# Performance work log

Hardware: AMD Instinct MI355X
Metric: run time of the kernel (lower is better)

The kernel has to match this reference:

```python
import jax, jax.numpy as jnp
import numpy as np

EMBED = 2048
HEADS = 16
HEAD_DIM = EMBED // HEADS
CHUNK = 128
BASE = 10000.0
EPS = 1e-6


def setup_inputs() -> dict:
    key = jax.random.key(0)
    ks = jax.random.split(key, 8)
    b, n, d = 2, 2048, EMBED
    std = 0.02
    return {
        "x": jax.random.normal(ks[0], (b, n, d), jnp.float32),
        "Wq": jax.random.normal(ks[1], (d, d), jnp.float32) * std,
        "Wk": jax.random.normal(ks[2], (d, d), jnp.float32) * std,
        "Wv": jax.random.normal(ks[3], (d, d), jnp.float32) * std,
        "Wo": jax.random.normal(ks[4], (d, d), jnp.float32) * std,
        "Wg1": jax.random.normal(ks[5], (d, HEAD_DIM), jnp.float32) * std,
        "Wg2": jax.random.normal(ks[6], (HEAD_DIM, d), jnp.float32) * std,
        "norm_weight": jnp.ones((d,), jnp.float32),
    }


def _alibi_log_decay(h):
    # lightning attention 'constant' decay: per-head ALiBi slope, log_lambda = -slope
    slopes = 2.0 ** (-8.0 * (jnp.arange(h, dtype=jnp.float32) + 1.0) / h)
    return -slopes  # [h]


def _lrpe_rotate(x):
    # RoPE-like rotation on head_dim (half-split), offset=0
    b, n, h, d = x.shape
    half = d // 2
    theta = BASE ** (-2.0 * jnp.arange(half, dtype=jnp.float32) / d)  # [half]
    ang = jnp.arange(n, dtype=jnp.float32)[:, None] * theta[None, :]  # [n, half]
    cos = jnp.cos(ang)[None, :, None, :]
    sin = jnp.sin(ang)[None, :, None, :]
    x1, x2 = x[..., :half], x[..., half:]
    return jnp.concatenate([x1 * cos - x2 * sin, x1 * sin + x2 * cos], axis=-1)


def _lightning_attn(q, k, v, log_lam):
    # chunk-recurrent linear attention with per-head exponential decay
    b, n, h, d = q.shape
    C = CHUNK
    nc = n // C
    qc = q.reshape(b, nc, C, h, d).transpose(1, 0, 2, 3, 4)  # [nc,b,C,h,d]
    kc = k.reshape(b, nc, C, h, d).transpose(1, 0, 2, 3, 4)
    vc = v.reshape(b, nc, C, h, d).transpose(1, 0, 2, 3, 4)
    i = jnp.arange(C, dtype=jnp.float32)
    diff = i[:, None] - i[None, :]  # [C,C]
    # intra-chunk decay mask D[h,t,s] = lambda_h^(t-s) for t>=s else 0
    D = jnp.where(diff[None] >= 0, jnp.exp(log_lam[:, None, None] * diff[None]), 0.0)
    decay_q = jnp.exp(log_lam[None, :] * (i[:, None] + 1.0))    # [C,h]
    decay_k = jnp.exp(log_lam[None, :] * (C - 1.0 - i[:, None]))  # [C,h]
    lam_C = jnp.exp(log_lam * C)  # [h]

    def step(S, qkv):
        qi, ki, vi = qkv  # [b,C,h,d]
        scores = jnp.einsum('bthd,bshd->bhts', qi, ki) * D[None]
        o_intra = jnp.einsum('bhts,bshd->bthd', scores, vi)
        o_inter = jnp.einsum('bthd,bhde->bthe', qi * decay_q[None, :, :, None], S)
        S_new = lam_C[None, :, None, None] * S + jnp.einsum(
            'bshd,bshe->bhde', ki * decay_k[None, :, :, None], vi)
        return S_new, o_intra + o_inter

    S0 = jnp.zeros((b, h, d, d), q.dtype)
    _, o = jax.lax.scan(step, S0, (qc, kc, vc))  # o: [nc,b,C,h,d]
    return o.transpose(1, 0, 2, 3, 4).reshape(b, n, h, d)


def _gated_group_rmsnorm(o, gate, weight):
    # gate_pos='pre', gate_act='sigmoid', num_groups=HEADS
    b, n, d = o.shape
    x = o * jax.nn.sigmoid(gate)
    xg = x.reshape(b, n, HEADS, HEAD_DIM)
    ms = jnp.mean(xg * xg, axis=-1, keepdims=True)
    xg = xg * jax.lax.rsqrt(ms + EPS)
    return xg.reshape(b, n, d) * weight


def reference(x, Wq, Wk, Wv, Wo, Wg1, Wg2, norm_weight):
    b, n, d = x.shape
    q = (x @ Wq).reshape(b, n, HEADS, HEAD_DIM)
    k = (x @ Wk).reshape(b, n, HEADS, HEAD_DIM)
    v = (x @ Wv).reshape(b, n, HEADS, HEAD_DIM)
    q = jax.nn.silu(q)
    k = jax.nn.silu(k)
    q = _lrpe_rotate(q)
    k = _lrpe_rotate(k)
    log_lam = _alibi_log_decay(HEADS)
    o = _lightning_attn(q, k, v, log_lam).reshape(b, n, d)
    gate = (x @ Wg1) @ Wg2
    o = _gated_group_rmsnorm(o, gate, norm_weight)
    return o @ Wo
```

## Files before the change

### kernel.cpp

```cpp
#include <hip/hip_runtime.h>


#define DEV __device__ __forceinline__
typedef unsigned short u16;
typedef __bf16 bf16x8 __attribute__((ext_vector_type(8)));
typedef float f32x4 __attribute__((ext_vector_type(4)));
typedef u16 u16x8 __attribute__((ext_vector_type(8)));

DEV u16 f2bf(float f) {
  unsigned u = __builtin_bit_cast(unsigned, f);
  u += 0x7fffu + ((u >> 16) & 1u);
  return (u16)(u >> 16);
}
DEV float bf2f(u16 h) {
  unsigned u = ((unsigned)h) << 16;
  return __builtin_bit_cast(float, u);
}
DEV void async16(const u16* g, u16* l) {
  __builtin_amdgcn_global_load_lds(
      (const __attribute__((address_space(1))) unsigned int*)g,
      (__attribute__((address_space(3))) unsigned int*)l, 16, 0, 0);
}

__global__ void convert_f32_bf16(const float* __restrict__ in, u16* __restrict__ out, long n) {
  long i = ((long)blockIdx.x * blockDim.x + threadIdx.x) * 4;
  if (i >= n) return;
  float4 v = *(const float4*)(in + i);
  ushort4 p;
  p.x = f2bf(v.x); p.y = f2bf(v.y); p.z = f2bf(v.z); p.w = f2bf(v.w);
  *(ushort4*)(out + i) = p;
}

__global__ void transpose_all(const float* __restrict__ Wq, const float* __restrict__ Wk,
                              const float* __restrict__ Wv, const float* __restrict__ Wo,
                              const float* __restrict__ Wg1, const float* __restrict__ Wg2,
                              u16* __restrict__ wtqkvg, u16* __restrict__ wot,
                              u16* __restrict__ wg2t) {
  __shared__ float t[32][33];
  int id = blockIdx.x;
  const float* in; u16* out; int K, N, bx, by;
  bool perm = false;
  if (id < 12288) {
    int w = id >> 12, tt = id & 4095;
    in = (w == 0) ? Wq : (w == 1) ? Wk : Wv;
    out = wtqkvg + (long)w * 2048 * 2048;
    K = 2048; N = 2048; bx = tt & 63; by = tt >> 6;
    perm = (w < 2);
  } else if (id < 16384) {
    int tt = id - 12288;
    in = Wo; out = wot; K = 2048; N = 2048; bx = tt & 63; by = tt >> 6;
  } else if (id < 16640) {
    int tt = id - 16384;
    in = Wg1; out = wtqkvg + 6144L * 2048; K = 2048; N = 128; bx = tt & 3; by = tt >> 2;
  } else {
    int tt = id - 16640;
    in = Wg2; out = wg2t; K = 128; N = 2048; bx = tt & 63; by = tt >> 6;
  }
  int c = threadIdx.x & 31, r0 = threadIdx.x >> 5;
  for (int r = r0; r < 32; r += 8)
    t[r][c] = in[(long)(by * 32 + r) * N + bx * 32 + c];
  __syncthreads();
  for (int r = r0; r < 32; r += 8) {
    int n = bx * 32 + r, nr = n;
    if (perm) {
      int h = n >> 7, j = n & 127, jj = j & 63, hi = j >> 6;
      nr = h * 128 + (jj & 15) + 32 * (jj >> 4) + 16 * hi;
    }
    out[(long)nr * K + by * 32 + c] = f2bf(t[c][r]);
  }
}

template <typename OutT>
__global__ __launch_bounds__(256, 2) void gemm_bt(
    const u16* __restrict__ A, const u16* __restrict__ B, OutT* __restrict__ C,
    int M, int N, int K, int lda, int ldb, int ldc, int rot,
    int nc, long sA1, long sA2, long sB1, long sB2, long sC1, long sC2) {
  __shared__ u16 sA[128 * 64], sB[128 * 64];
  {
    int z = blockIdx.z, z1 = z / nc, z2 = z % nc;
    A += z1 * sA1 + z2 * sA2;
    B += z1 * sB1 + z2 * sB2;
    C += z1 * sC1 + z2 * sC2;
  }
  const int tid = threadIdx.x, lane = tid & 63, wid = tid >> 6;
  const int bm = blockIdx.y * 128, bn = blockIdx.x * 128;
  const int ch0 = wid * 2, ch1 = ch0 + 1;
  const int lr = lane >> 2;
  const int ak = (((lane & 3) - ((lane >> 3) & 3)) & 3) * 8;
  const int ar0 = ch0 * 16 + lr, ar1 = ch1 * 16 + lr;
  const u16* gA0 = A + (long)(bm + ar0) * lda + ak;
  const u16* gA1 = A + (long)(bm + ar1) * lda + ak;
  const u16* gB0 = B + (long)(bn + ar0) * ldb + ak;
  const u16* gB1 = B + (long)(bn + ar1) * ldb + ak;
  u16* lA0 = sA + ch0 * 512; u16* lA1 = sA + ch1 * 512;
  u16* lB0 = sB + ch0 * 512; u16* lB1 = sB + ch1 * 512;
  const int wm = (wid & 1) * 64, wn = (wid >> 1) * 64;
  const int fm = lane & 15, kq = lane >> 4;
  const int qs = ((kq + (fm >> 1)) & 3) * 8;
  const int aoff = (wm >> 4) * 512 + fm * 32 + qs;
  const int boff = (wn >> 4) * 512 + fm * 32 + qs;
  f32x4 acc[4][4] = {};
  for (int kb = 0; kb < K; kb += 64) {
    async16(gA0, lA0); async16(gA1, lA1);
    async16(gB0, lB0); async16(gB1, lB1);
    async16(gA0 + 32, lA0 + 4096); async16(gA1 + 32, lA1 + 4096);
    async16(gB0 + 32, lB0 + 4096); async16(gB1 + 32, lB1 + 4096);
    gA0 += 64; gA1 += 64; gB0 += 64; gB1 += 64;
    __syncthreads();
#pragma unroll
    for (int half = 0; half < 2; half++) {
      const int ho = half * 4096;
      bf16x8 af[4], bfr[4];
#pragma unroll
      for (int i = 0; i < 4; i++) af[i] = *(const bf16x8*)&sA[ho + aoff + i * 512];
#pragma unroll
      for (int i = 0; i < 4; i++) bfr[i] = *(const bf16x8*)&sB[ho + boff + i * 512];
#pragma unroll
      for (int mt = 0; mt < 4; mt++)
#pragma unroll
        for (int nt = 0; nt < 4; nt++)
          acc[mt][nt] = __builtin_amdgcn_mfma_f32_16x16x32_bf16(af[mt], bfr[nt], acc[mt][nt], 0, 0, 0);
    }
    __syncthreads();
  }
  const int cr = (lane >> 4) * 4;
  if constexpr (sizeof(OutT) == 2) {
    if (rot && bn < 4096) {
#pragma unroll
      for (int mt = 0; mt < 4; mt++)
#pragma unroll
        for (int r = 0; r < 4; r++) {
          long row = bm + wm + mt * 16 + cr + r;
          float tf = (float)(int)(row & 2047);
#pragma unroll
          for (int np = 0; np < 4; np += 2) {
            float x1 = acc[mt][np][r], x2 = acc[mt][np + 1][r];
            x1 = x1 / (1.f + __expf(-x1));
            x2 = x2 / (1.f + __expf(-x2));
            int jj = fm + 16 * ((wn >> 5) + (np >> 1));
            float th = exp2f(-13.287712379549449f * (float)jj * (1.f / 64.f));
            float ang = tf * th;
            float sn = __sinf(ang), cs = __cosf(ang);
            C[row * ldc + bn + jj]      = f2bf(x1 * cs - x2 * sn);
            C[row * ldc + bn + 64 + jj] = f2bf(x1 * sn + x2 * cs);
          }
        }
      return;
    }
  }
#pragma unroll
  for (int mt = 0; mt < 4; mt++)
#pragma unroll
    for (int nt = 0; nt < 4; nt++)
#pragma unroll
      for (int r = 0; r < 4; r++) {
        long row = bm + wm + mt * 16 + cr + r;
        long col = bn + wn + nt * 16 + fm;
        float v = acc[mt][nt][r];
        if constexpr (sizeof(OutT) == 2) C[row * ldc + col] = f2bf(v);
        else                             C[row * ldc + col] = v;
      }
}

__global__ void transpose_kv(const u16* __restrict__ qkv, u16* __restrict__ kdT,
                             u16* __restrict__ vT) {
  __shared__ float t[32][33];
  int z = blockIdx.z, which = z >> 5, bh = z & 31;
  int b = bh >> 4, h = bh & 15;
  u16* out = which ? vT : kdT;
  int slab = which ? 2 : 1, decay = which ? 0 : 1;
  int n0 = blockIdx.x * 32, d0 = blockIdx.y * 32;
  int cc = threadIdx.x & 31, rr0 = threadIdx.x >> 5;
  float log_lam = -exp2f(-0.5f * (float)(h + 1));
  for (int rr = rr0; rr < 32; rr += 8) {
    int n = n0 + rr;
    float v = bf2f(qkv[(long)(b * 2048 + n) * 6272 + slab * 2048 + h * 128 + d0 + cc]);
    if (decay) v *= expf(log_lam * (float)(127 - (n & 127)));
    t[rr][cc] = v;
  }
  __syncthreads();
  for (int rr = rr0; rr < 32; rr += 8)
    out[((long)bh * 128 + d0 + rr) * 2048 + n0 + cc] = f2bf(t[cc][rr]);
}

__global__ void scan_state(const u16* __restrict__ U, u16* __restrict__ S_all) {
  int blk = blockIdx.x;
  int bh = blk >> 3, sl = blk & 7, h = bh & 15;
  float log_lam = -exp2f(-0.5f * (float)(h + 1));
  float lamC = expf(log_lam * 128.f);
  long off = (long)bh * 16 * 16384 + sl * 2048 + threadIdx.x * 8;
  float s[8];
#pragma unroll
  for (int j = 0; j < 8; j++) s[j] = 0.f;
  for (int c = 0; c < 16; c++) {
    long idx = off + (long)c * 16384;
    u16x8 sb;
#pragma unroll
    for (int j = 0; j < 8; j++) sb[j] = f2bf(s[j]);
    *(u16x8*)(S_all + idx) = sb;
    u16x8 ub = *(const u16x8*)(U + idx);
#pragma unroll
    for (int j = 0; j < 8; j++) s[j] = lamC * s[j] + bf2f(ub[j]);
  }
}

__global__ __launch_bounds__(256, 1) void attn_out(
    const u16* __restrict__ qkv, const u16* __restrict__ vT,
    const u16* __restrict__ S_all, const u16* __restrict__ gate,
    const float* __restrict__ nw, u16* __restrict__ nrm) {
  __shared__ u16 sA[128 * 32], sB[128 * 32], sK[128 * 32];
  __shared__ u16 sS[128 * 136];
  __shared__ float sNorm[2][128];
  const int blk = blockIdx.x;
  const int bh = blk >> 4, c = blk & 15;
  const int b = bh >> 4, h = bh & 15;
  const float log_lam = -exp2f(-0.5f * (float)(h + 1));
  const int tid = threadIdx.x, lane = tid & 63, wid = tid >> 6;
  const int wm = (wid & 1) * 64, wn = (wid >> 1) * 64;
  const int fm = lane & 15, fq = lane >> 4, kq = lane >> 4;
  const int lr = lane >> 2;
  const int ak = (((lane & 3) - ((lane >> 3) & 3)) & 3) * 8;
  const int ch0 = wid * 2, ch1 = ch0 + 1;
  const int r0 = ch0 * 16 + lr, r1 = ch1 * 16 + lr;
  const int qs = ((kq + (fm >> 1)) & 3) * 8;
  const int aoff = (wm >> 4) * 512 + fm * 32 + qs;
  const int boff = (wn >> 4) * 512 + fm * 32 + qs;
  const u16* qbase = qkv + (long)(b * 2048 + c * 128) * 6272 + h * 128;
  const u16* kbase = qbase + 2048;
  const u16* Sbase = S_all + ((long)bh * 16 + c) * 16384;
  const u16* vbase = vT + (long)bh * 262144 + (long)c * 128;

  f32x4 acc[4][4] = {};
  f32x4 sc[4][4] = {};
  for (int kb = 0; kb < 128; kb += 32) {
    async16(qbase + (long)r0 * 6272 + kb + ak, sA + ch0 * 512);
    async16(qbase + (long)r1 * 6272 + kb + ak, sA + ch1 * 512);
    async16(Sbase + r0 * 128 + kb + ak, sB + ch0 * 512);
    async16(Sbase + r1 * 128 + kb + ak, sB + ch1 * 512);
    async16(kbase + (long)r0 * 6272 + kb + ak, sK + ch0 * 512);
    async16(kbase + (long)r1 * 6272 + kb + ak, sK + ch1 * 512);
    __syncthreads();
    bf16x8 aq[4], bs[4], bk[4];
#pragma unroll
    for (int i = 0; i < 4; i++) {
      aq[i] = *(const bf16x8*)&sA[aoff + i * 512];
      bs[i] = *(const bf16x8*)&sB[boff + i * 512];
      bk[i] = *(const bf16x8*)&sK[boff + i * 512];
    }
#pragma unroll
    for (int mt = 0; mt < 4; mt++)
#pragma unroll
      for (int nt = 0; nt < 4; nt++) {
        acc[mt][nt] = __builtin_amdgcn_mfma_f32_16x16x32_bf16(aq[mt], bs[nt], acc[mt][nt], 0, 0, 0);
        sc[mt][nt] = __builtin_amdgcn_mfma_f32_16x16x32_bf16(aq[mt], bk[nt], sc[mt][nt], 0, 0, 0);
      }
    __syncthreads();
  }
#pragma unroll
  for (int mt = 0; mt < 4; mt++)
#pragma unroll
    for (int r = 0; r < 4; r++) {
      int t = wm + mt * 16 + fq * 4 + r;
      float d = expf(log_lam * (float)(t + 1));
#pragma unroll
      for (int nt = 0; nt < 4; nt++) acc[mt][nt][r] *= d;
    }
#pragma unroll
  for (int mt = 0; mt < 4; mt++)
#pragma unroll
    for (int nt = 0; nt < 4; nt++)
#pragma unroll
      for (int r = 0; r < 4; r++) {
        int t = wm + mt * 16 + fq * 4 + r;
        int s = wn + nt * 16 + fm;
        float v = sc[mt][nt][r];
        v = (t >= s) ? v * expf(log_lam * (float)(t - s)) : 0.f;
        sS[t * 136 + s] = f2bf(v);
      }
  __syncthreads();
  for (int kb = 0; kb < 128; kb += 32) {
    async16(vbase + r0 * 2048 + kb + ak, sB + ch0 * 512);
    async16(vbase + r1 * 2048 + kb + ak, sB + ch1 * 512);
    __syncthreads();
    bf16x8 as[4], bv[4];
#pragma unroll
    for (int i = 0; i < 4; i++) {
      as[i] = *(const bf16x8*)&sS[(wm + i * 16 + fm) * 136 + kb + kq * 8];
      bv[i] = *(const bf16x8*)&sB[boff + i * 512];
    }
#pragma unroll
    for (int mt = 0; mt < 4; mt++)
#pragma unroll
      for (int nt = 0; nt < 4; nt++)
        acc[mt][nt] = __builtin_amdgcn_mfma_f32_16x16x32_bf16(as[mt], bv[nt], acc[mt][nt], 0, 0, 0);
    __syncthreads();
  }
  const u16* gbase = gate + (long)(b * 2048 + c * 128) * 2048 + h * 128;
  float nwv[4];
#pragma unroll
  for (int nt = 0; nt < 4; nt++) nwv[nt] = nw[h * 128 + wn + nt * 16 + fm];
  float part[4][4];
#pragma unroll
  for (int mt = 0; mt < 4; mt++)
#pragma unroll
    for (int r = 0; r < 4; r++) {
      int t = wm + mt * 16 + fq * 4 + r;
      float p = 0.f;
#pragma unroll
      for (int nt = 0; nt < 4; nt++) {
        int e = wn + nt * 16 + fm;
        float g = bf2f(gbase[(long)t * 2048 + e]);
        float x = acc[mt][nt][r] / (1.f + __expf(-g));
        acc[mt][nt][r] = x;
        p += x * x;
      }
      part[mt][r] = p;
    }
#pragma unroll
  for (int o = 1; o < 16; o <<= 1)
#pragma unroll
    for (int mt = 0; mt < 4; mt++)
#pragma unroll
      for (int r = 0; r < 4; r++) part[mt][r] += __shfl_xor(part[mt][r], o);
  if (fm == 0) {
#pragma unroll
    for (int mt = 0; mt < 4; mt++)
#pragma unroll
      for (int r = 0; r < 4; r++)
        sNorm[wid >> 1][wm + mt * 16 + fq * 4 + r] = part[mt][r];
  }
  __syncthreads();
  long orow0 = (long)(b * 2048 + c * 128);
#pragma unroll
  for (int mt = 0; mt < 4; mt++)
#pragma unroll
    for (int r = 0; r < 4; r++) {
      int t = wm + mt * 16 + fq * 4 + r;
      float ms = (sNorm[0][t] + sNorm[1][t]) * (1.f / 128.f);
      float rs = rsqrtf(ms + 1e-6f);
#pragma unroll
      for (int nt = 0; nt < 4; nt++) {
        int e = wn + nt * 16 + fm;
        nrm[(orow0 + t) * 2048 + h * 128 + e] = f2bf(acc[mt][nt][r] * rs * nwv[nt]);
      }
    }
}

extern "C" void kernel_launch(void* const* d_in, const int* in_sizes, int n_in,
                              void* d_out, int out_size, void* d_ws, size_t ws_size,
                              hipStream_t stream) {
  (void)in_sizes; (void)n_in; (void)out_size; (void)ws_size;
  const float* x   = (const float*)d_in[0];
  const float* Wq  = (const float*)d_in[1];
  const float* Wk  = (const float*)d_in[2];
  const float* Wv  = (const float*)d_in[3];
  const float* Wo  = (const float*)d_in[4];
  const float* Wg1 = (const float*)d_in[5];
  const float* Wg2 = (const float*)d_in[6];
  const float* nw  = (const float*)d_in[7];
  float* out = (float*)d_out;

  char* ws = (char*)d_ws;
  size_t off = 0;
  auto alloc = [&](size_t bytes) -> void* {
    void* p = ws + off;
    off += (bytes + 255) & ~(size_t)255;
    return p;
  };
  u16* xb    = (u16*)alloc(4096UL * 2048 * 2);
  u16* wtqkv = (u16*)alloc(6272UL * 2048 * 2);
  u16* wot   = (u16*)alloc(2048UL * 2048 * 2);
  u16* wg2t  = (u16*)alloc(2048UL * 128 * 2);
  u16* qkvg  = (u16*)alloc(4096UL * 6272 * 2);
  u16* gate  = (u16*)alloc(4096UL * 2048 * 2);
  u16* kdT   = (u16*)alloc(32UL * 128 * 2048 * 2);
  u16* vT    = (u16*)alloc(32UL * 128 * 2048 * 2);
  u16* Ubuf  = (u16*)alloc(512UL * 16384 * 2);
  u16* S_all = (u16*)alloc(512UL * 16384 * 2);
  u16* nrm   = (u16*)alloc(4096UL * 2048 * 2);

  convert_f32_bf16<<<dim3(8192), dim3(256), 0, stream>>>(x, xb, 8388608L);
  transpose_all<<<dim3(16896), dim3(256), 0, stream>>>(Wq, Wk, Wv, Wo, Wg1, Wg2,
                                                       wtqkv, wot, wg2t);
  gemm_bt<u16><<<dim3(49, 32, 1), dim3(256), 0, stream>>>(xb, wtqkv, qkvg,
      4096, 6272, 2048, 2048, 2048, 6272, 1, 1, 0, 0, 0, 0, 0, 0);
  gemm_bt<u16><<<dim3(16, 32, 1), dim3(256), 0, stream>>>(qkvg + 6144, wg2t, gate,
      4096, 2048, 128, 6272, 128, 2048, 0, 1, 0, 0, 0, 0, 0, 0);
  transpose_kv<<<dim3(64, 4, 64), dim3(256), 0, stream>>>(qkvg, kdT, vT);
  gemm_bt<u16><<<dim3(1, 1, 512), dim3(256), 0, stream>>>(vT, kdT, Ubuf,
      128, 128, 128, 2048, 2048, 128, 0,
      16, 262144L, 128L, 262144L, 128L, 262144L, 16384L);
  scan_state<<<dim3(256), dim3(256), 0, stream>>>(Ubuf, S_all);
  attn_out<<<dim3(512), dim3(256), 0, stream>>>(qkvg, vT, S_all, gate, nw, nrm);
  gemm_bt<float><<<dim3(16, 32, 1), dim3(256), 0, stream>>>(nrm, wot, out,
      4096, 2048, 2048, 2048, 2048, 2048, 0, 1, 0, 0, 0, 0, 0, 0);
}
```

Measured before the change: 437.2 us.

## Fuse gate up-projection GEMM into attn_out and shrink gemm K-tile

Removes the separate gate GEMM, which wrote a 4096x2048 bf16 gate buffer. attn_out now computes the gate tile itself, multiplying the 128-wide gate-down activations in qkvg by the per-head slice of Wg2 with MFMA before the sigmoid and RMSNorm. This drops one launch and the gate buffer's write and read, at the cost of a little extra compute inside attn_out. Separately, gemm_bt's K-step goes from 64 to 32, halving shared memory per block but doubling the loop iterations and barriers in the large QKV and output GEMMs.

```diff
diff --git a/kernel.cpp b/kernel.cpp
--- a/kernel.cpp
+++ b/kernel.cpp
@@ -75,7 +75,7 @@
     const u16* __restrict__ A, const u16* __restrict__ B, OutT* __restrict__ C,
     int M, int N, int K, int lda, int ldb, int ldc, int rot,
     int nc, long sA1, long sA2, long sB1, long sB2, long sC1, long sC2) {
-  __shared__ u16 sA[128 * 64], sB[128 * 64];
+  __shared__ u16 sA[128 * 32], sB[128 * 32];
   {
     int z = blockIdx.z, z1 = z / nc, z2 = z % nc;
     A += z1 * sA1 + z2 * sA2;
@@ -100,27 +100,21 @@
   const int aoff = (wm >> 4) * 512 + fm * 32 + qs;
   const int boff = (wn >> 4) * 512 + fm * 32 + qs;
   f32x4 acc[4][4] = {};
-  for (int kb = 0; kb < K; kb += 64) {
+  for (int kb = 0; kb < K; kb += 32) {
     async16(gA0, lA0); async16(gA1, lA1);
     async16(gB0, lB0); async16(gB1, lB1);
-    async16(gA0 + 32, lA0 + 4096); async16(gA1 + 32, lA1 + 4096);
-    async16(gB0 + 32, lB0 + 4096); async16(gB1 + 32, lB1 + 4096);
-    gA0 += 64; gA1 += 64; gB0 += 64; gB1 += 64;
-    __syncthreads();
-#pragma unroll
-    for (int half = 0; half < 2; half++) {
-      const int ho = half * 4096;
-      bf16x8 af[4], bfr[4];
-#pragma unroll
-      for (int i = 0; i < 4; i++) af[i] = *(const bf16x8*)&sA[ho + aoff + i * 512];
-#pragma unroll
-      for (int i = 0; i < 4; i++) bfr[i] = *(const bf16x8*)&sB[ho + boff + i * 512];
-#pragma unroll
-      for (int mt = 0; mt < 4; mt++)
-#pragma unroll
-        for (int nt = 0; nt < 4; nt++)
-          acc[mt][nt] = __builtin_amdgcn_mfma_f32_16x16x32_bf16(af[mt], bfr[nt], acc[mt][nt], 0, 0, 0);
-    }
+    gA0 += 32; gA1 += 32; gB0 += 32; gB1 += 32;
+    __syncthreads();
+    bf16x8 af[4], bfr[4];
+#pragma unroll
+    for (int i = 0; i < 4; i++) af[i] = *(const bf16x8*)&sA[aoff + i * 512];
+#pragma unroll
+    for (int i = 0; i < 4; i++) bfr[i] = *(const bf16x8*)&sB[boff + i * 512];
+#pragma unroll
+    for (int mt = 0; mt < 4; mt++)
+#pragma unroll
+      for (int nt = 0; nt < 4; nt++)
+        acc[mt][nt] = __builtin_amdgcn_mfma_f32_16x16x32_bf16(af[mt], bfr[nt], acc[mt][nt], 0, 0, 0);
     __syncthreads();
   }
   const int cr = (lane >> 4) * 4;
@@ -206,7 +200,7 @@
 
 __global__ __launch_bounds__(256, 1) void attn_out(
     const u16* __restrict__ qkv, const u16* __restrict__ vT,
-    const u16* __restrict__ S_all, const u16* __restrict__ gate,
+    const u16* __restrict__ S_all, const u16* __restrict__ wg2t,
     const float* __restrict__ nw, u16* __restrict__ nrm) {
   __shared__ u16 sA[128 * 32], sB[128 * 32], sK[128 * 32];
   __shared__ u16 sS[128 * 136];
@@ -295,7 +289,28 @@
         acc[mt][nt] = __builtin_amdgcn_mfma_f32_16x16x32_bf16(as[mt], bv[nt], acc[mt][nt], 0, 0, 0);
     __syncthreads();
   }
-  const u16* gbase = gate + (long)(b * 2048 + c * 128) * 2048 + h * 128;
+  const u16* gbase = qkv + (long)(b * 2048 + c * 128) * 6272 + 6144;
+  const u16* wbase = wg2t + (long)h * 128 * 128;
+  f32x4 gacc[4][4] = {};
+  for (int kb = 0; kb < 128; kb += 32) {
+    async16(gbase + (long)r0 * 6272 + kb + ak, sA + ch0 * 512);
+    async16(gbase + (long)r1 * 6272 + kb + ak, sA + ch1 * 512);
+    async16(wbase + r0 * 128 + kb + ak, sK + ch0 * 512);
+    async16(wbase + r1 * 128 + kb + ak, sK + ch1 * 512);
+    __syncthreads();
+    bf16x8 ag[4], bw[4];
+#pragma unroll
+    for (int i = 0; i < 4; i++) {
+      ag[i] = *(const bf16x8*)&sA[aoff + i * 512];
+      bw[i] = *(const bf16x8*)&sK[boff + i * 512];
+    }
+#pragma unroll
+    for (int mt = 0; mt < 4; mt++)
+#pragma unroll
+      for (int nt = 0; nt < 4; nt++)
+        gacc[mt][nt] = __builtin_amdgcn_mfma_f32_16x16x32_bf16(ag[mt], bw[nt], gacc[mt][nt], 0, 0, 0);
+    __syncthreads();
+  }
   float nwv[4];
 #pragma unroll
   for (int nt = 0; nt < 4; nt++) nwv[nt] = nw[h * 128 + wn + nt * 16 + fm];
@@ -304,13 +319,10 @@
   for (int mt = 0; mt < 4; mt++)
 #pragma unroll
     for (int r = 0; r < 4; r++) {
-      int t = wm + mt * 16 + fq * 4 + r;
       float p = 0.f;
 #pragma unroll
       for (int nt = 0; nt < 4; nt++) {
-        int e = wn + nt * 16 + fm;
-        float g = bf2f(gbase[(long)t * 2048 + e]);
-        float x = acc[mt][nt][r] / (1.f + __expf(-g));
+        float x = acc[mt][nt][r] / (1.f + __expf(-gacc[mt][nt][r]));
         acc[mt][nt][r] = x;
         p += x * x;
       }
@@ -372,7 +384,6 @@
   u16* wot   = (u16*)alloc(2048UL * 2048 * 2);
   u16* wg2t  = (u16*)alloc(2048UL * 128 * 2);
   u16* qkvg  = (u16*)alloc(4096UL * 6272 * 2);
-  u16* gate  = (u16*)alloc(4096UL * 2048 * 2);
   u16* kdT   = (u16*)alloc(32UL * 128 * 2048 * 2);
   u16* vT    = (u16*)alloc(32UL * 128 * 2048 * 2);
   u16* Ubuf  = (u16*)alloc(512UL * 16384 * 2);
@@ -384,14 +395,12 @@
                                                        wtqkv, wot, wg2t);
   gemm_bt<u16><<<dim3(49, 32, 1), dim3(256), 0, stream>>>(xb, wtqkv, qkvg,
       4096, 6272, 2048, 2048, 2048, 6272, 1, 1, 0, 0, 0, 0, 0, 0);
-  gemm_bt<u16><<<dim3(16, 32, 1), dim3(256), 0, stream>>>(qkvg + 6144, wg2t, gate,
-      4096, 2048, 128, 6272, 128, 2048, 0, 1, 0, 0, 0, 0, 0, 0);
   transpose_kv<<<dim3(64, 4, 64), dim3(256), 0, stream>>>(qkvg, kdT, vT);
   gemm_bt<u16><<<dim3(1, 1, 512), dim3(256), 0, stream>>>(vT, kdT, Ubuf,
       128, 128, 128, 2048, 2048, 128, 0,
       16, 262144L, 128L, 262144L, 128L, 262144L, 16384L);
   scan_state<<<dim3(256), dim3(256), 0, stream>>>(Ubuf, S_all);
-  attn_out<<<dim3(512), dim3(256), 0, stream>>>(qkvg, vT, S_all, gate, nw, nrm);
+  attn_out<<<dim3(512), dim3(256), 0, stream>>>(qkvg, vT, S_all, wg2t, nw, nrm);
   gemm_bt<float><<<dim3(16, 32, 1), dim3(256), 0, stream>>>(nrm, wot, out,
       4096, 2048, 2048, 2048, 2048, 2048, 0, 1, 0, 0, 0, 0, 0, 0);
 }
```

Measured after the change: 427.5 us. -2.2%, faster.
